# Optimization experiments

Hardware: AMD Instinct MI355X
Metric: run time of the kernel (lower is better)

The kernel has to match this reference:

```python
import jax, jax.numpy as jnp
import numpy as np

EPS = 1e-7
N = 100000
E = 1600000
IN_DIM = 128
OUT_DIM = 128


def _norm(t):
    # clamped L2 norm over last dim, keepdims
    return jnp.clip(jnp.linalg.norm(t, axis=-1, keepdims=True), EPS, None)


def log_map_zero(x, c):
    sqrt_c = jnp.sqrt(c)
    xn = _norm(x)
    y = jnp.clip(sqrt_c * xn, None, 1.0 - 1e-5)
    return jnp.arctanh(y) * x / (sqrt_c * xn)


def exp_map_zero(v, c):
    sqrt_c = jnp.sqrt(c)
    vn = _norm(v)
    return jnp.tanh(sqrt_c * vn) * v / (sqrt_c * vn)


def setup_inputs() -> dict:
    key = jax.random.key(0)
    k1, k2, k3, k4 = jax.random.split(key, 4)
    x = 0.1 * jax.random.normal(k1, (N, IN_DIM), dtype=jnp.float32)  # inside ball
    edge_index = jax.random.randint(k2, (2, E), 0, N, dtype=jnp.int64)
    c = jnp.ones((), dtype=jnp.float32)
    # Xavier-uniform weight (out_dim, in_dim)
    limit = float(np.sqrt(6.0 / (IN_DIM + OUT_DIM)))
    weight = jax.random.uniform(k3, (OUT_DIM, IN_DIM), minval=-limit, maxval=limit, dtype=jnp.float32)
    bias = jnp.zeros((OUT_DIM,), dtype=jnp.float32)
    return {"x": x, "edge_index": edge_index, "c": c, "num_nodes": N,
            "weight": weight, "bias": bias}


def reference(x, edge_index, c, num_nodes, weight, bias):
    # 1. log-map all node features to tangent space at origin
    v = log_map_zero(x, c)  # (N, in_dim)
    src, dst = edge_index[0], edge_index[1]
    # 2. mean aggregation over neighbours (incl. self) via segment_sum
    agg = jax.ops.segment_sum(v[src], dst, num_segments=num_nodes) + v
    count = jax.ops.segment_sum(jnp.ones((src.shape[0],), dtype=v.dtype), dst,
                                num_segments=num_nodes) + 1.0
    v_agg = agg / jnp.clip(count, 1.0, None)[:, None]
    # 3. back to hyperbolic space, then hyperbolic linear
    x_hyp = exp_map_zero(v_agg, c)
    v2 = log_map_zero(x_hyp, c)
    out = v2 @ weight.T + bias
    return exp_map_zero(out, c)
```

## Files before the change

### kernel.cpp

```cpp
#include <hip/hip_runtime.h>
#include <math.h>

#define EPSF 1e-7f
#define YMAXF 0.99999f
#define WPITCH 136

#define NBUCK 256
#define PB_CHUNK 2048

typedef short bf16x8 __attribute__((ext_vector_type(8)));
typedef short bf16x4 __attribute__((ext_vector_type(4)));
typedef float f32x4  __attribute__((ext_vector_type(4)));
typedef int   i32x4  __attribute__((ext_vector_type(4)));

__device__ __forceinline__ float grp32_sum(float v) {
    v += __shfl_xor(v, 1);
    v += __shfl_xor(v, 2);
    v += __shfl_xor(v, 4);
    v += __shfl_xor(v, 8);
    v += __shfl_xor(v, 16);
    return v;
}

__device__ __forceinline__ short f2bf(float f) {
    unsigned u = __float_as_uint(f);
    unsigned r = (u + 0x7FFFu + ((u >> 16) & 1u)) >> 16;
    return (short)r;
}

__device__ __forceinline__ float bf_lo(int w) {
    return __uint_as_float(((unsigned)w) << 16);
}
__device__ __forceinline__ float bf_hi(int w) {
    return __uint_as_float(((unsigned)w) & 0xffff0000u);
}

__global__ __launch_bounds__(256)
void logmap_kernel(const float* __restrict__ x,
                   const float* __restrict__ c_ptr,
                   short* __restrict__ v_bf,
                   const float* __restrict__ W,
                   short* __restrict__ W_bf,
                   int* __restrict__ bucketCount,
                   int N) {
    int gid = blockIdx.x * blockDim.x + threadIdx.x;
    if (gid < NBUCK) bucketCount[gid] = 0;
    if (gid < 4096) {
        float4 w4 = ((const float4*)W)[gid];
        bf16x4 w;
        w[0] = f2bf(w4.x); w[1] = f2bf(w4.y); w[2] = f2bf(w4.z); w[3] = f2bf(w4.w);
        *(bf16x4*)&W_bf[gid * 4] = w;
    }
    int row = gid >> 5;
    if (row >= N) return;
    int lane = gid & 31;
    const float4 xv = ((const float4*)x)[(size_t)row * 32 + lane];
    float ss = xv.x * xv.x + xv.y * xv.y + xv.z * xv.z + xv.w * xv.w;
    ss = grp32_sum(ss);
    float sc = sqrtf(c_ptr[0]);
    float xn = fmaxf(sqrtf(ss), EPSF);
    float y = fminf(sc * xn, YMAXF);
    float s = atanhf(y) / (sc * xn);
    bf16x4 pk;
    pk[0] = f2bf(s * xv.x); pk[1] = f2bf(s * xv.y);
    pk[2] = f2bf(s * xv.z); pk[3] = f2bf(s * xv.w);
    *(bf16x4*)&v_bf[(size_t)row * 128 + lane * 4] = pk;
}

__global__ __launch_bounds__(256)
void bucket_count_kernel(const int* __restrict__ eidx_dst,
                         int* __restrict__ bucketCount, int E) {
    __shared__ int h[NBUCK];
    int tid = threadIdx.x;
    h[tid] = 0;
    __syncthreads();
    int per = (E + gridDim.x - 1) / gridDim.x;
    int start = blockIdx.x * per;
    int end = min(start + per, E);
    for (int i = start + tid; i < end; i += 256)
        atomicAdd(&h[eidx_dst[i] >> 9], 1);
    __syncthreads();
    if (h[tid]) atomicAdd(&bucketCount[tid], h[tid]);
}

__global__ __launch_bounds__(256)
void bucket_scan_kernel(const int* __restrict__ bucketCount,
                        int* __restrict__ bucket_base,
                        int* __restrict__ cursor) {
    __shared__ int part[256];
    int tid = threadIdx.x;
    int val = bucketCount[tid];
    part[tid] = val;
    __syncthreads();
    for (int off = 1; off < 256; off <<= 1) {
        int t = (tid >= off) ? part[tid - off] : 0;
        __syncthreads();
        part[tid] += t;
        __syncthreads();
    }
    int excl = part[tid] - val;
    bucket_base[tid] = excl;
    cursor[tid] = excl;
}

__global__ __launch_bounds__(256)
void bucket_scatter_kernel(const int* __restrict__ eidx,
                           int* __restrict__ cursor,
                           int* __restrict__ bucketed, int E) {
    __shared__ int hist[NBUCK];
    __shared__ int lstart[NBUCK];
    __shared__ int gbase[NBUCK];
    __shared__ int part[256];
    __shared__ int stage[PB_CHUNK];
    __shared__ unsigned char stageB[PB_CHUNK];

    int tid = threadIdx.x;
    int start = blockIdx.x * PB_CHUNK;
    int cnt = min(PB_CHUNK, E - start);
    hist[tid] = 0;
    __syncthreads();

    const int J = PB_CHUNK / 256;
    int myP[J], myB[J], myR[J];
    #pragma unroll
    for (int j = 0; j < J; ++j) {
        int idx = j * 256 + tid;
        myR[j] = -1;
        if (idx < cnt) {
            int e = start + idx;
            int d = eidx[E + e];
            int s = eidx[e];
            int b = d >> 9;
            myB[j] = b;
            myP[j] = ((d & 511) << 17) | s;
            myR[j] = atomicAdd(&hist[b], 1);
        }
    }
    __syncthreads();
    part[tid] = hist[tid];
    __syncthreads();
    for (int off = 1; off < 256; off <<= 1) {
        int t = (tid >= off) ? part[tid - off] : 0;
        __syncthreads();
        part[tid] += t;
        __syncthreads();
    }
    lstart[tid] = part[tid] - hist[tid];
    if (hist[tid]) gbase[tid] = atomicAdd(&cursor[tid], hist[tid]);
    __syncthreads();
    #pragma unroll
    for (int j = 0; j < J; ++j) {
        if (myR[j] >= 0) {
            int pos = lstart[myB[j]] + myR[j];
            stage[pos] = myP[j];
            stageB[pos] = (unsigned char)myB[j];
        }
    }
    __syncthreads();
    for (int i = tid; i < cnt; i += 256) {
        int b = stageB[i];
        bucketed[gbase[b] + (i - lstart[b])] = stage[i];
    }
}

__global__ __launch_bounds__(256)
void csr_kernel(const int* __restrict__ bucketed,
                const int* __restrict__ bucket_base,
                const int* __restrict__ cursor_post,
                int* __restrict__ offsets, int* __restrict__ deg,
                int* __restrict__ sorted_src, int N) {
    __shared__ int hist[512];
    __shared__ int pre[512];
    __shared__ int cur[512];
    __shared__ int part[256];
    int b = blockIdx.x;
    int tid = threadIdx.x;
    int start = bucket_base[b];
    int end = cursor_post[b];
    hist[tid] = 0;
    hist[tid + 256] = 0;
    __syncthreads();
    for (int i = start + tid; i < end; i += 256)
        atomicAdd(&hist[bucketed[i] >> 17], 1);
    __syncthreads();
    int a0 = hist[2 * tid], a1 = hist[2 * tid + 1];
    part[tid] = a0 + a1;
    __syncthreads();
    for (int off = 1; off < 256; off <<= 1) {
        int t = (tid >= off) ? part[tid - off] : 0;
        __syncthreads();
        part[tid] += t;
        __syncthreads();
    }
    int base2 = part[tid] - (a0 + a1);
    pre[2 * tid] = base2;
    pre[2 * tid + 1] = base2 + a0;
    cur[2 * tid] = base2;
    cur[2 * tid + 1] = base2 + a0;
    __syncthreads();
    int node0 = b << 9;
    for (int i = tid; i < 512; i += 256) {
        int node = node0 + i;
        if (node < N) { offsets[node] = start + pre[i]; deg[node] = hist[i]; }
    }
    for (int i = start + tid; i < end; i += 256) {
        int p = bucketed[i];
        int ld = p >> 17;
        int src = p & 0x1FFFF;
        int r = atomicAdd(&cur[ld], 1);
        sorted_src[start + r] = src;
    }
}

__global__ __launch_bounds__(256, 4)
void gather_epilogue_kernel(const short* __restrict__ v_bf,
                            const int* __restrict__ sorted_src,
                            const int* __restrict__ offsets,
                            const int* __restrict__ deg,
                            const short* __restrict__ W_bf,
                            const float* __restrict__ bias,
                            const float* __restrict__ c_ptr,
                            float* __restrict__ out,
                            int N) {
    __shared__ short v2l[64 * WPITCH];

    int tid = threadIdx.x;
    int wave = tid >> 6;
    int lane = tid & 63;
    int quad = lane >> 4;
    int l16  = lane & 15;
    int g  = tid >> 4;
    int gl = tid & 15;
    float sc = sqrtf(c_ptr[0]);

    float bsv[8];
    #pragma unroll
    for (int c = 0; c < 8; ++c) bsv[c] = bias[c * 16 + l16];

    int row_base = blockIdx.x * 64;

    int offs[4], degs[4];
    #pragma unroll
    for (int t = 0; t < 4; ++t) {
        int row = row_base + t * 16 + g;
        bool valid = (row < N);
        offs[t] = valid ? offsets[row] : 0;
        degs[t] = valid ? deg[row] : 0;
    }

    for (int t = 0; t < 4; ++t) {
        int row = row_base + t * 16 + g;
        bool valid = (row < N);
        float acc[8];
        #pragma unroll
        for (int i = 0; i < 8; ++i) acc[i] = 0.0f;
        int start = offs[t], d = degs[t];
        if (valid) {
            bf16x8 r0 = *(const bf16x8*)&v_bf[(size_t)row * 128 + gl * 8];
            i32x4 w0 = *(const i32x4*)&r0;
            #pragma unroll
            for (int k2 = 0; k2 < 4; ++k2) {
                acc[2 * k2]     = bf_lo(w0[k2]);
                acc[2 * k2 + 1] = bf_hi(w0[k2]);
            }
        }
        int batch = (d > 0) ? sorted_src[start + min(gl, d - 1)] : 0;
        for (int j = 0; j < d; j += 16) {
            int m = d - j;
            int nb = (j + 16 < d) ? sorted_src[start + min(j + 16 + gl, d - 1)] : 0;

            bf16x8 q0, q1, q2, q3, q4, q5, q6, q7,
                   q8, q9, qA, qB, qC, qD, qE, qF;
            __builtin_amdgcn_sched_barrier(0);
#define GLD(i, dst) do {                                                      \
        int src_ = __shfl(batch, (lane & 48) | (i));                          \
        unsigned voff_ = ((unsigned)src_ << 8) | (unsigned)(gl << 4);         \
        asm volatile("global_load_dwordx4 %0, %1, %2"                         \
                     : "=v"(dst) : "v"(voff_), "s"(v_bf));                    \
    } while (0)
            GLD(0, q0);  GLD(1, q1);  GLD(2, q2);  GLD(3, q3);
            GLD(4, q4);  GLD(5, q5);  GLD(6, q6);  GLD(7, q7);
            GLD(8, q8);  GLD(9, q9);  GLD(10, qA); GLD(11, qB);
            GLD(12, qC); GLD(13, qD); GLD(14, qE); GLD(15, qF);
#undef GLD
            asm volatile("s_waitcnt vmcnt(8)" ::: "memory");
            __builtin_amdgcn_sched_barrier(0);

#define ACC(i, rsrc) do {                                                     \
        float w_ = ((i) < m) ? 1.0f : 0.0f;                                   \
        i32x4 wv_ = *(i32x4*)&(rsrc);                                         \
        acc[0] = fmaf(bf_lo(wv_[0]), w_, acc[0]);                             \
        acc[1] = fmaf(bf_hi(wv_[0]), w_, acc[1]);                             \
        acc[2] = fmaf(bf_lo(wv_[1]), w_, acc[2]);                             \
        acc[3] = fmaf(bf_hi(wv_[1]), w_, acc[3]);                             \
        acc[4] = fmaf(bf_lo(wv_[2]), w_, acc[4]);                             \
        acc[5] = fmaf(bf_hi(wv_[2]), w_, acc[5]);                             \
        acc[6] = fmaf(bf_lo(wv_[3]), w_, acc[6]);                             \
        acc[7] = fmaf(bf_hi(wv_[3]), w_, acc[7]);                             \
    } while (0)
            ACC(0, q0);  ACC(1, q1);  ACC(2, q2);  ACC(3, q3);
            ACC(4, q4);  ACC(5, q5);  ACC(6, q6);  ACC(7, q7);
            asm volatile("s_waitcnt vmcnt(0)" ::: "memory");
            __builtin_amdgcn_sched_barrier(0);
            ACC(8, q8);  ACC(9, q9);  ACC(10, qA); ACC(11, qB);
            ACC(12, qC); ACC(13, qD); ACC(14, qE); ACC(15, qF);
#undef ACC
            batch = nb;
        }
        float inv = 1.0f / (float)(d + 1);
        #pragma unroll
        for (int i = 0; i < 8; ++i) acc[i] *= inv;

        float ss = 0.0f;
        #pragma unroll
        for (int i = 0; i < 8; ++i) ss += acc[i] * acc[i];
        ss += __shfl_xor(ss, 1);
        ss += __shfl_xor(ss, 2);
        ss += __shfl_xor(ss, 4);
        ss += __shfl_xor(ss, 8);

        float vn  = sqrtf(ss);
        float vnc = fmaxf(vn, EPSF);
        float th  = tanhf(sc * vnc);
        float tt  = th / (sc * vnc);
        float hn  = fmaxf(th / sc, EPSF);
        float y2  = fminf(sc * hn, YMAXF);
        float s2  = atanhf(y2) / (sc * hn);
        float scale = s2 * tt;

        bf16x8 pk;
        #pragma unroll
        for (int i = 0; i < 8; ++i) pk[i] = f2bf(acc[i] * scale);
        *(bf16x8*)&v2l[(t * 16 + g) * WPITCH + gl * 8] = pk;
    }
    __syncthreads();

    f32x4 acc2[8];
    #pragma unroll
    for (int c = 0; c < 8; ++c) acc2[c] = (f32x4){bsv[c], bsv[c], bsv[c], bsv[c]};
    #pragma unroll
    for (int k0 = 0; k0 < 128; k0 += 32) {
        bf16x8 af = *(const bf16x8*)&v2l[(wave * 16 + l16) * WPITCH + k0 + quad * 8];
        #pragma unroll
        for (int c = 0; c < 8; ++c) {
            bf16x8 bw = *(const bf16x8*)&W_bf[(c * 16 + l16) * 128 + k0 + quad * 8];
            acc2[c] = __builtin_amdgcn_mfma_f32_16x16x32_bf16(af, bw, acc2[c], 0, 0, 0);
        }
    }

    #pragma unroll
    for (int r = 0; r < 4; ++r) {
        float ss = 0.0f;
        #pragma unroll
        for (int c = 0; c < 8; ++c) ss += acc2[c][r] * acc2[c][r];
        ss += __shfl_xor(ss, 1);
        ss += __shfl_xor(ss, 2);
        ss += __shfl_xor(ss, 4);
        ss += __shfl_xor(ss, 8);
        float on  = sqrtf(ss);
        float onc = fmaxf(on, EPSF);
        float gsc = tanhf(sc * onc) / (sc * onc);
        int orow = row_base + wave * 16 + quad * 4 + r;
        if (orow < N) {
            size_t base = (size_t)orow * 128;
            #pragma unroll
            for (int c = 0; c < 8; ++c)
                out[base + c * 16 + l16] = gsc * acc2[c][r];
        }
    }
}

extern "C" void kernel_launch(void* const* d_in, const int* in_sizes, int n_in,
                              void* d_out, int out_size, void* d_ws, size_t ws_size,
                              hipStream_t stream) {
    const float* x     = (const float*)d_in[0];
    const int*   eidx  = (const int*)d_in[1];
    const float* c_ptr = (const float*)d_in[2];
    const float* W     = (const float*)d_in[4];
    const float* bias  = (const float*)d_in[5];
    float* out = (float*)d_out;

    int N = in_sizes[0] / 128;
    int E = in_sizes[1] / 2;

    short* v_bf        = (short*)d_ws;
    int*   deg         = (int*)(v_bf + (size_t)N * 128);
    int*   offsets     = deg + N;
    int*   bucketCount = offsets + N;
    int*   bucket_base = bucketCount + NBUCK;
    int*   cursor      = bucket_base + NBUCK;
    short* W_bf        = (short*)(cursor + NBUCK);
    int*   bucketed    = (int*)(W_bf + 128 * 128);
    int*   sorted_src  = bucketed + E;

    {
        long long threads = (long long)N * 32;
        int blocks = (int)((threads + 255) / 256);
        hipLaunchKernelGGL(logmap_kernel, dim3(blocks), dim3(256), 0, stream,
                           x, c_ptr, v_bf, W, W_bf, bucketCount, N);
    }
    hipLaunchKernelGGL(bucket_count_kernel, dim3(256), dim3(256), 0, stream,
                       eidx + E, bucketCount, E);
    hipLaunchKernelGGL(bucket_scan_kernel, dim3(1), dim3(256), 0, stream,
                       bucketCount, bucket_base, cursor);
    {
        int blocks = (E + PB_CHUNK - 1) / PB_CHUNK;
        hipLaunchKernelGGL(bucket_scatter_kernel, dim3(blocks), dim3(256), 0, stream,
                           eidx, cursor, bucketed, E);
    }
    {
        int blocks = (N + 511) / 512;
        hipLaunchKernelGGL(csr_kernel, dim3(blocks), dim3(256), 0, stream,
                           bucketed, bucket_base, cursor, offsets, deg, sorted_src, N);
    }
    {
        int blocks = (N + 63) / 64;
        hipLaunchKernelGGL(gather_epilogue_kernel, dim3(blocks), dim3(256), 0, stream,
                           v_bf, sorted_src, offsets, deg, W_bf, bias, c_ptr, out, N);
    }
}
```

Before: 271.5 us.

## Use finer dst buckets, fold bucket counting into logmap, shrink gather blocks

Destination buckets grow from 256 to 1024, each now covering 128 nodes instead of 512. The scans and the CSR kernel are reworked to match, and the CSR pass now gets many more blocks. The separate bucket-count kernel is removed: logmap now does the counting with global atomics, and a memset clears the counters. This saves a launch but drops the shared-memory privatization, so many threads contend on the same global counters. The gather/epilogue kernel moves to 128-thread blocks of 32 rows, aiming for better occupancy and load balance.

```diff
diff --git a/kernel.cpp b/kernel.cpp
--- a/kernel.cpp
+++ b/kernel.cpp
@@ -5,7 +5,7 @@
 #define YMAXF 0.99999f
 #define WPITCH 136
 
-#define NBUCK 256
+#define NBUCK 1024
 #define PB_CHUNK 2048
 
 typedef short bf16x8 __attribute__((ext_vector_type(8)));
@@ -41,16 +41,17 @@
                    short* __restrict__ v_bf,
                    const float* __restrict__ W,
                    short* __restrict__ W_bf,
+                   const int* __restrict__ eidx_dst,
                    int* __restrict__ bucketCount,
-                   int N) {
+                   int N, int E) {
     int gid = blockIdx.x * blockDim.x + threadIdx.x;
-    if (gid < NBUCK) bucketCount[gid] = 0;
     if (gid < 4096) {
         float4 w4 = ((const float4*)W)[gid];
         bf16x4 w;
         w[0] = f2bf(w4.x); w[1] = f2bf(w4.y); w[2] = f2bf(w4.z); w[3] = f2bf(w4.w);
         *(bf16x4*)&W_bf[gid * 4] = w;
     }
+    if (gid < E) atomicAdd(&bucketCount[eidx_dst[gid] >> 7], 1);
     int row = gid >> 5;
     if (row >= N) return;
     int lane = gid & 31;
@@ -68,29 +69,16 @@
 }
 
 __global__ __launch_bounds__(256)
-void bucket_count_kernel(const int* __restrict__ eidx_dst,
-                         int* __restrict__ bucketCount, int E) {
-    __shared__ int h[NBUCK];
-    int tid = threadIdx.x;
-    h[tid] = 0;
-    __syncthreads();
-    int per = (E + gridDim.x - 1) / gridDim.x;
-    int start = blockIdx.x * per;
-    int end = min(start + per, E);
-    for (int i = start + tid; i < end; i += 256)
-        atomicAdd(&h[eidx_dst[i] >> 9], 1);
-    __syncthreads();
-    if (h[tid]) atomicAdd(&bucketCount[tid], h[tid]);
-}
-
-__global__ __launch_bounds__(256)
 void bucket_scan_kernel(const int* __restrict__ bucketCount,
                         int* __restrict__ bucket_base,
                         int* __restrict__ cursor) {
     __shared__ int part[256];
     int tid = threadIdx.x;
-    int val = bucketCount[tid];
-    part[tid] = val;
+    int v[4];
+    int s = 0;
+    #pragma unroll
+    for (int j = 0; j < 4; ++j) { v[j] = bucketCount[tid * 4 + j]; s += v[j]; }
+    part[tid] = s;
     __syncthreads();
     for (int off = 1; off < 256; off <<= 1) {
         int t = (tid >= off) ? part[tid - off] : 0;
@@ -98,9 +86,14 @@
         part[tid] += t;
         __syncthreads();
     }
-    int excl = part[tid] - val;
-    bucket_base[tid] = excl;
-    cursor[tid] = excl;
+    int run = part[tid] - s;
+    #pragma unroll
+    for (int j = 0; j < 4; ++j) {
+        int b = tid * 4 + j;
+        bucket_base[b] = run;
+        cursor[b] = run;
+        run += v[j];
+    }
 }
 
 __global__ __launch_bounds__(256)
@@ -112,12 +105,13 @@
     __shared__ int gbase[NBUCK];
     __shared__ int part[256];
     __shared__ int stage[PB_CHUNK];
-    __shared__ unsigned char stageB[PB_CHUNK];
+    __shared__ unsigned short stageB[PB_CHUNK];
 
     int tid = threadIdx.x;
     int start = blockIdx.x * PB_CHUNK;
     int cnt = min(PB_CHUNK, E - start);
-    hist[tid] = 0;
+    #pragma unroll
+    for (int j = 0; j < 4; ++j) hist[tid * 4 + j] = 0;
     __syncthreads();
 
     const int J = PB_CHUNK / 256;
@@ -130,14 +124,18 @@
             int e = start + idx;
             int d = eidx[E + e];
             int s = eidx[e];
-            int b = d >> 9;
+            int b = d >> 7;
             myB[j] = b;
-            myP[j] = ((d & 511) << 17) | s;
+            myP[j] = ((d & 127) << 17) | s;
             myR[j] = atomicAdd(&hist[b], 1);
         }
     }
     __syncthreads();
-    part[tid] = hist[tid];
+    int h4[4];
+    int tsum = 0;
+    #pragma unroll
+    for (int j = 0; j < 4; ++j) { h4[j] = hist[tid * 4 + j]; tsum += h4[j]; }
+    part[tid] = tsum;
     __syncthreads();
     for (int off = 1; off < 256; off <<= 1) {
         int t = (tid >= off) ? part[tid - off] : 0;
@@ -145,15 +143,21 @@
         part[tid] += t;
         __syncthreads();
     }
-    lstart[tid] = part[tid] - hist[tid];
-    if (hist[tid]) gbase[tid] = atomicAdd(&cursor[tid], hist[tid]);
+    int run = part[tid] - tsum;
+    #pragma unroll
+    for (int j = 0; j < 4; ++j) {
+        int b = tid * 4 + j;
+        lstart[b] = run;
+        if (h4[j]) gbase[b] = atomicAdd(&cursor[b], h4[j]);
+        run += h4[j];
+    }
     __syncthreads();
     #pragma unroll
     for (int j = 0; j < J; ++j) {
         if (myR[j] >= 0) {
             int pos = lstart[myB[j]] + myR[j];
             stage[pos] = myP[j];
-            stageB[pos] = (unsigned char)myB[j];
+            stageB[pos] = (unsigned short)myB[j];
         }
     }
     __syncthreads();
@@ -169,40 +173,34 @@
                 const int* __restrict__ cursor_post,
                 int* __restrict__ offsets, int* __restrict__ deg,
                 int* __restrict__ sorted_src, int N) {
-    __shared__ int hist[512];
-    __shared__ int pre[512];
-    __shared__ int cur[512];
-    __shared__ int part[256];
+    __shared__ int hist[128];
+    __shared__ int cur[128];
+    __shared__ int part[128];
     int b = blockIdx.x;
     int tid = threadIdx.x;
     int start = bucket_base[b];
     int end = cursor_post[b];
-    hist[tid] = 0;
-    hist[tid + 256] = 0;
+    if (tid < 128) hist[tid] = 0;
     __syncthreads();
     for (int i = start + tid; i < end; i += 256)
         atomicAdd(&hist[bucketed[i] >> 17], 1);
     __syncthreads();
-    int a0 = hist[2 * tid], a1 = hist[2 * tid + 1];
-    part[tid] = a0 + a1;
-    __syncthreads();
-    for (int off = 1; off < 256; off <<= 1) {
-        int t = (tid >= off) ? part[tid - off] : 0;
-        __syncthreads();
-        part[tid] += t;
-        __syncthreads();
-    }
-    int base2 = part[tid] - (a0 + a1);
-    pre[2 * tid] = base2;
-    pre[2 * tid + 1] = base2 + a0;
-    cur[2 * tid] = base2;
-    cur[2 * tid + 1] = base2 + a0;
-    __syncthreads();
-    int node0 = b << 9;
-    for (int i = tid; i < 512; i += 256) {
-        int node = node0 + i;
-        if (node < N) { offsets[node] = start + pre[i]; deg[node] = hist[i]; }
-    }
+    int h = (tid < 128) ? hist[tid] : 0;
+    if (tid < 128) part[tid] = h;
+    __syncthreads();
+    for (int off = 1; off < 128; off <<= 1) {
+        int t = (tid < 128 && tid >= off) ? part[tid - off] : 0;
+        __syncthreads();
+        if (tid < 128) part[tid] += t;
+        __syncthreads();
+    }
+    if (tid < 128) {
+        int excl = part[tid] - h;
+        cur[tid] = excl;
+        int node = (b << 7) + tid;
+        if (node < N) { offsets[node] = start + excl; deg[node] = h; }
+    }
+    __syncthreads();
     for (int i = start + tid; i < end; i += 256) {
         int p = bucketed[i];
         int ld = p >> 17;
@@ -212,7 +210,7 @@
     }
 }
 
-__global__ __launch_bounds__(256, 4)
+__global__ __launch_bounds__(128, 6)
 void gather_epilogue_kernel(const short* __restrict__ v_bf,
                             const int* __restrict__ sorted_src,
                             const int* __restrict__ offsets,
@@ -222,7 +220,7 @@
                             const float* __restrict__ c_ptr,
                             float* __restrict__ out,
                             int N) {
-    __shared__ short v2l[64 * WPITCH];
+    __shared__ short v2l[32 * WPITCH];
 
     int tid = threadIdx.x;
     int wave = tid >> 6;
@@ -237,19 +235,19 @@
     #pragma unroll
     for (int c = 0; c < 8; ++c) bsv[c] = bias[c * 16 + l16];
 
-    int row_base = blockIdx.x * 64;
+    int row_base = blockIdx.x * 32;
 
     int offs[4], degs[4];
     #pragma unroll
     for (int t = 0; t < 4; ++t) {
-        int row = row_base + t * 16 + g;
+        int row = row_base + t * 8 + g;
         bool valid = (row < N);
         offs[t] = valid ? offsets[row] : 0;
         degs[t] = valid ? deg[row] : 0;
     }
 
     for (int t = 0; t < 4; ++t) {
-        int row = row_base + t * 16 + g;
+        int row = row_base + t * 8 + g;
         bool valid = (row < N);
         float acc[8];
         #pragma unroll
@@ -331,7 +329,7 @@
         bf16x8 pk;
         #pragma unroll
         for (int i = 0; i < 8; ++i) pk[i] = f2bf(acc[i] * scale);
-        *(bf16x8*)&v2l[(t * 16 + g) * WPITCH + gl * 8] = pk;
+        *(bf16x8*)&v2l[(t * 8 + g) * WPITCH + gl * 8] = pk;
     }
     __syncthreads();
 
@@ -393,14 +391,14 @@
     int*   bucketed    = (int*)(W_bf + 128 * 128);
     int*   sorted_src  = bucketed + E;
 
+    hipMemsetAsync(bucketCount, 0, NBUCK * sizeof(int), stream);
+
     {
         long long threads = (long long)N * 32;
         int blocks = (int)((threads + 255) / 256);
         hipLaunchKernelGGL(logmap_kernel, dim3(blocks), dim3(256), 0, stream,
-                           x, c_ptr, v_bf, W, W_bf, bucketCount, N);
-    }
-    hipLaunchKernelGGL(bucket_count_kernel, dim3(256), dim3(256), 0, stream,
-                       eidx + E, bucketCount, E);
+                           x, c_ptr, v_bf, W, W_bf, eidx + E, bucketCount, N, E);
+    }
     hipLaunchKernelGGL(bucket_scan_kernel, dim3(1), dim3(256), 0, stream,
                        bucketCount, bucket_base, cursor);
     {
@@ -409,13 +407,13 @@
                            eidx, cursor, bucketed, E);
     }
     {
-        int blocks = (N + 511) / 512;
+        int blocks = (N + 127) / 128;
         hipLaunchKernelGGL(csr_kernel, dim3(blocks), dim3(256), 0, stream,
                            bucketed, bucket_base, cursor, offsets, deg, sorted_src, N);
     }
     {
-        int blocks = (N + 63) / 64;
-        hipLaunchKernelGGL(gather_epilogue_kernel, dim3(blocks), dim3(256), 0, stream,
+        int blocks = (N + 31) / 32;
+        hipLaunchKernelGGL(gather_epilogue_kernel, dim3(blocks), dim3(128), 0, stream,
                            v_bf, sorted_src, offsets, deg, W_bf, bias, c_ptr, out, N);
     }
 }
```

After: 801.4 us. +195.2%, slower.
